# Kernel optimization log

Measured on AMD Instinct MI355X. Metric: run time of the kernel, lower is better.

Reference implementation:

```python
import jax, jax.numpy as jnp
import numpy as np


def setup_inputs() -> dict:
    key = jax.random.key(0)
    k1, k2, k3, k4, k5 = jax.random.split(key, 5)
    B, C, H, W = 8, 32, 64, 64
    inp = jax.random.normal(k1, (B, C, H, W), dtype=jnp.float32)
    # expected positions lie inside the image grid
    exPx = jax.random.uniform(k2, (B, H, W), dtype=jnp.float32) * (W - 1)
    exPy = jax.random.uniform(k3, (B, H, W), dtype=jnp.float32) * (H - 1)
    # positive Gaussian widths in roughly [1, 3]
    sigmax = jax.random.uniform(k4, (B, H, W), dtype=jnp.float32) * 2.0 + 1.0
    sigmay = jax.random.uniform(k5, (B, H, W), dtype=jnp.float32) * 2.0 + 1.0
    return {"input": inp, "exPx": exPx, "exPy": exPy,
            "sigmax": sigmax, "sigmay": sigmay}


def reference(input, exPx, exPy, sigmax, sigmay):
    """Gaussian-weighted spatial swap/warp (soft gather).

    For each output pixel (i, j):
      out[b,c,i,j] = sum_{u,v} G(u; exPy[b,i,j], sigmay[b,i,j])
                              * G(v; exPx[b,i,j], sigmax[b,i,j])
                              * input[b,c,u,v]  /  Z[b,i,j]
    where G is an unnormalized Gaussian and Z is the total weight mass.
    The 2D Gaussian weight is separable, so we contract rows then cols.
    """
    B, C, H, W = input.shape
    u = jnp.arange(H, dtype=input.dtype)  # source row coords (y)
    v = jnp.arange(W, dtype=input.dtype)  # source col coords (x)
    # wy: [B,H,W,H] weight over source rows u for each output pixel (i,j)
    wy = jnp.exp(-0.5 * ((u[None, None, None, :] - exPy[..., None]) / sigmay[..., None]) ** 2)
    # wx: [B,H,W,W] weight over source cols v
    wx = jnp.exp(-0.5 * ((v[None, None, None, :] - exPx[..., None]) / sigmax[..., None]) ** 2)
    # normalization mass per output pixel
    Z = wy.sum(-1) * wx.sum(-1) + jnp.asarray(1e-8, input.dtype)  # [B,H,W]
    # contract over source rows u -> [B,C,H,W,W]
    t = jnp.einsum('biju,bcuv->bcijv', wy, input)
    # contract over source cols v -> [B,C,H,W]
    out = jnp.einsum('bcijv,bijv->bcij', t, wx)
    return out / Z[:, None]
```

## Files before the change

### kernel.cpp

```cpp
#include <hip/hip_runtime.h>


#define BB 8
#define CC 32
#define HH 64
#define WW 64

typedef __attribute__((ext_vector_type(8))) short short8;
typedef __attribute__((ext_vector_type(4))) float f32x4;
typedef unsigned int uint;

__device__ __forceinline__ uint rn_bf16(float f) {
    uint u = __float_as_uint(f);
    return (u + 0x7FFFu + ((u >> 16) & 1u)) >> 16;
}

__global__ void preconvert_kernel(const float* __restrict__ x, uint* __restrict__ hi)
{
    const int n = BB * CC * HH * WW / 2;
    int idx = blockIdx.x * blockDim.x + threadIdx.x;
    for (; idx < n; idx += gridDim.x * blockDim.x) {
        const float2 d = ((const float2*)x)[idx];
        hi[idx] = rn_bf16(d.x) | (rn_bf16(d.y) << 16);
    }
}

#define WYB_OFF   0
#define WXH_OFF   8704
#define SUM_OFF   17920
#define INVZ_OFF  19968
#define LDS_BYTES 20224
#define RED_OFF   0

__global__ __launch_bounds__(256, 6)
void swap_mfma_kernel(const uint* __restrict__ xhi,
                      const float* __restrict__ exPx, const float* __restrict__ exPy,
                      const float* __restrict__ sigmax, const float* __restrict__ sigmay,
                      float* __restrict__ out)
{
    __shared__ __align__(16) char lds[LDS_BYTES];
    const int t    = threadIdx.x;
    const int lane = t & 63;
    const int w    = t >> 6;
    const int q    = (t >> 4) & 3;
    const int ln   = t & 15;
    const int bid   = blockIdx.x;
    const int b     = bid & 7;
    const int r     = bid >> 3;
    const int chalf = r & 1;
    const int i     = r >> 1;
    const int bi    = b * 64 + i;

    {
        const int p = lane;
        const int g = w;
        const int pixBase = bi * 64 + p;
        const float ey = exPy[pixBase], ex = exPx[pixBase];
        const float isy = 1.0f / sigmay[pixBase], isx = 1.0f / sigmax[pixBase];
        float sy = 0.0f, sx = 0.0f;
        uint* WYB = (uint*)(lds + WYB_OFF);
        #pragma unroll
        for (int j = 0; j < 8; ++j) {
            const int u0 = g * 16 + 2 * j;
            const float dy0 = ((float)u0       - ey) * isy;
            const float dy1 = ((float)(u0 + 1) - ey) * isy;
            const float wy0 = __expf(-0.5f * dy0 * dy0);
            const float wy1 = __expf(-0.5f * dy1 * dy1);
            sy += wy0 + wy1;
            WYB[p * 34 + g * 8 + j] = rn_bf16(wy0) | (rn_bf16(wy1) << 16);
        }
        uint* WXH = (uint*)(lds + WXH_OFF);
        #pragma unroll
        for (int j = 0; j < 8; ++j) {
            const int v0 = g * 16 + 2 * j;
            const float dx0 = ((float)v0       - ex) * isx;
            const float dx1 = ((float)(v0 + 1) - ex) * isx;
            const float wx0 = __expf(-0.5f * dx0 * dx0);
            const float wx1 = __expf(-0.5f * dx1 * dx1);
            sx += wx0 + wx1;
            WXH[p * 36 + g * 8 + j] = rn_bf16(wx0) | (rn_bf16(wx1) << 16);
        }
        float* SUMY = (float*)(lds + SUM_OFF);
        float* SUMX = SUMY + 256;
        SUMY[g * 64 + p] = sy;
        SUMX[g * 64 + p] = sx;
    }
    __syncthreads();
    float* INVZ = (float*)(lds + INVZ_OFF);
    if (t < 64) {
        float* SUMY = (float*)(lds + SUM_OFF);
        float* SUMX = SUMY + 256;
        const float sy = SUMY[t] + SUMY[64 + t] + SUMY[128 + t] + SUMY[192 + t];
        const float sx = SUMX[t] + SUMX[64 + t] + SUMX[128 + t] + SUMX[192 + t];
        INVZ[t] = 1.0f / (sy * sx + 1e-8f);
    }
    __syncthreads();

    short8 bh[4][2];
    #pragma unroll
    for (int nt = 0; nt < 4; ++nt)
        #pragma unroll
        for (int ks = 0; ks < 2; ++ks)
            bh[nt][ks] = *(const short8*)(lds + WXH_OFF + (nt * 16 + ln) * 144 + ks * 64 + q * 16);
    float wyz[4][4];
    #pragma unroll
    for (int nt = 0; nt < 4; ++nt) {
        const int pp = nt * 16 + ln;
        const float iz = INVZ[pp];
        const uint2 wv = *(const uint2*)((const uint*)(lds + WYB_OFF) + pp * 34 + w * 8 + q * 2);
        wyz[nt][0] = __uint_as_float(wv.x << 16)          * iz;
        wyz[nt][1] = __uint_as_float(wv.x & 0xFFFF0000u)  * iz;
        wyz[nt][2] = __uint_as_float(wv.y << 16)          * iz;
        wyz[nt][3] = __uint_as_float(wv.y & 0xFFFF0000u)  * iz;
    }
    __syncthreads();

    const int cbase = b * CC + chalf * 16;
    float* RED = (float*)(lds + RED_OFF);
    const uint* xrow = xhi + (size_t)cbase * 2048 + (w * 16 + ln) * 32 + q * 4;

    #pragma unroll 4
    for (int c = 0; c < 16; ++c) {
        const uint4* src = (const uint4*)(xrow + (size_t)c * 2048);
        union { uint4 v; short8 s; } A0, A1;
        A0.v = src[0];
        A1.v = src[4];

        f32x4 acc[4];
        #pragma unroll
        for (int nt = 0; nt < 4; ++nt) acc[nt] = (f32x4){0.f, 0.f, 0.f, 0.f};
        #pragma unroll
        for (int nt = 0; nt < 4; ++nt) {
            acc[nt] = __builtin_amdgcn_mfma_f32_16x16x32_bf16(A0.s, bh[nt][0], acc[nt], 0, 0, 0);
            acc[nt] = __builtin_amdgcn_mfma_f32_16x16x32_bf16(A1.s, bh[nt][1], acc[nt], 0, 0, 0);
        }
        #pragma unroll
        for (int nt = 0; nt < 4; ++nt) {
            float ps = acc[nt][0] * wyz[nt][0] + acc[nt][1] * wyz[nt][1]
                     + acc[nt][2] * wyz[nt][2] + acc[nt][3] * wyz[nt][3];
            ps += __shfl_xor(ps, 16, 64);
            ps += __shfl_xor(ps, 32, 64);
            if (q == 0) RED[c * 256 + w * 64 + nt * 16 + ln] = ps;
        }
    }
    __syncthreads();

    {
        const int kk = t >> 6, p = t & 63;
        #pragma unroll
        for (int g = 0; g < 4; ++g) {
            const int c = g * 4 + kk;
            const float* Rk = RED + c * 256;
            const float o = Rk[p] + Rk[64 + p] + Rk[128 + p] + Rk[192 + p];
            out[(size_t)(cbase + c) * (HH * WW) + i * 64 + p] = o;
        }
    }
}

__device__ __forceinline__ void split_pair(float f0, float f1, uint& hi, uint& lo) {
    const uint u0 = __float_as_uint(f0), u1 = __float_as_uint(f1);
    hi = (u0 >> 16) | (u1 & 0xFFFF0000u);
    const float l0 = f0 - __uint_as_float(u0 & 0xFFFF0000u);
    const float l1 = f1 - __uint_as_float(u1 & 0xFFFF0000u);
    lo = (__float_as_uint(l0) >> 16) | (__float_as_uint(l1) & 0xFFFF0000u);
}

#define FB_WYS_OFF   0
#define FB_WXH_OFF   16640
#define FB_SUM_OFF   25856
#define FB_INVZ_OFF  27904
#define FB_LDS_BYTES 28160
#define FB_RED_OFF   0

__global__ __launch_bounds__(256, 4)
void swap_fused_kernel(const float* __restrict__ inp,
                       const float* __restrict__ exPx, const float* __restrict__ exPy,
                       const float* __restrict__ sigmax, const float* __restrict__ sigmay,
                       float* __restrict__ out)
{
    __shared__ __align__(16) char lds[FB_LDS_BYTES];
    const int t = threadIdx.x;
    const int lane = t & 63, w = t >> 6, q = (t >> 4) & 3, ln = t & 15;
    const int bid = blockIdx.x;
    const int b = bid & 7, r = bid >> 3;
    const int chalf = r & 1, i = r >> 1;
    const int bi = b * 64 + i;

    float* WYS = (float*)(lds + FB_WYS_OFF);
    {
        const int p = lane, g = w;
        const int pixBase = bi * 64 + p;
        const float ey = exPy[pixBase], ex = exPx[pixBase];
        const float isy = 1.0f / sigmay[pixBase], isx = 1.0f / sigmax[pixBase];
        float sy = 0.0f, sx = 0.0f;
        #pragma unroll
        for (int k = 0; k < 16; ++k) {
            const int u = g * 16 + k;
            const float dy = ((float)u - ey) * isy;
            const float wy = __expf(-0.5f * dy * dy);
            WYS[u * 65 + p] = wy; sy += wy;
        }
        uint* WXH = (uint*)(lds + FB_WXH_OFF);
        #pragma unroll
        for (int j = 0; j < 8; ++j) {
            const int v0 = g * 16 + 2 * j;
            const float dx0 = ((float)v0 - ex) * isx;
            const float dx1 = ((float)(v0 + 1) - ex) * isx;
            const float wx0 = __expf(-0.5f * dx0 * dx0);
            const float wx1 = __expf(-0.5f * dx1 * dx1);
            sx += wx0 + wx1;
            WXH[p * 36 + g * 8 + j] = rn_bf16(wx0) | (rn_bf16(wx1) << 16);
        }
        float* SUMY = (float*)(lds + FB_SUM_OFF);
        float* SUMX = SUMY + 256;
        SUMY[g * 64 + p] = sy; SUMX[g * 64 + p] = sx;
    }
    __syncthreads();
    float* INVZ = (float*)(lds + FB_INVZ_OFF);
    if (t < 64) {
        float* SUMY = (float*)(lds + FB_SUM_OFF);
        float* SUMX = SUMY + 256;
        const float sy = SUMY[t] + SUMY[64 + t] + SUMY[128 + t] + SUMY[192 + t];
        const float sx = SUMX[t] + SUMX[64 + t] + SUMX[128 + t] + SUMX[192 + t];
        INVZ[t] = 1.0f / (sy * sx + 1e-8f);
    }
    __syncthreads();
    short8 bh[4][2];
    #pragma unroll
    for (int nt = 0; nt < 4; ++nt)
        #pragma unroll
        for (int ks = 0; ks < 2; ++ks)
            bh[nt][ks] = *(const short8*)(lds + FB_WXH_OFF + (nt * 16 + ln) * 144 + ks * 64 + q * 16);
    float wyz[4][4];
    #pragma unroll
    for (int nt = 0; nt < 4; ++nt) {
        const float iz = INVZ[nt * 16 + ln];
        #pragma unroll
        for (int rr = 0; rr < 4; ++rr)
            wyz[nt][rr] = WYS[(w * 16 + q * 4 + rr) * 65 + nt * 16 + ln] * iz;
    }
    __syncthreads();
    const int cbase = b * CC + chalf * 16;
    float* RED = (float*)(lds + FB_RED_OFF);
    const float* xrow = inp + (size_t)cbase * 4096 + (w * 16 + ln) * 64 + q * 8;
    #pragma unroll 2
    for (int c = 0; c < 16; ++c) {
        const float4* src = (const float4*)(xrow + (size_t)c * 4096);
        const float4 x0 = src[0], x1 = src[1], x2 = src[8], x3 = src[9];
        union { uint u[4]; short8 s; } Ah0, Al0, Ah1, Al1;
        split_pair(x0.x, x0.y, Ah0.u[0], Al0.u[0]);
        split_pair(x0.z, x0.w, Ah0.u[1], Al0.u[1]);
        split_pair(x1.x, x1.y, Ah0.u[2], Al0.u[2]);
        split_pair(x1.z, x1.w, Ah0.u[3], Al0.u[3]);
        split_pair(x2.x, x2.y, Ah1.u[0], Al1.u[0]);
        split_pair(x2.z, x2.w, Ah1.u[1], Al1.u[1]);
        split_pair(x3.x, x3.y, Ah1.u[2], Al1.u[2]);
        split_pair(x3.z, x3.w, Ah1.u[3], Al1.u[3]);
        f32x4 acc[4];
        #pragma unroll
        for (int nt = 0; nt < 4; ++nt) acc[nt] = (f32x4){0.f, 0.f, 0.f, 0.f};
        #pragma unroll
        for (int nt = 0; nt < 4; ++nt) {
            acc[nt] = __builtin_amdgcn_mfma_f32_16x16x32_bf16(Ah0.s, bh[nt][0], acc[nt], 0, 0, 0);
            acc[nt] = __builtin_amdgcn_mfma_f32_16x16x32_bf16(Al0.s, bh[nt][0], acc[nt], 0, 0, 0);
            acc[nt] = __builtin_amdgcn_mfma_f32_16x16x32_bf16(Ah1.s, bh[nt][1], acc[nt], 0, 0, 0);
            acc[nt] = __builtin_amdgcn_mfma_f32_16x16x32_bf16(Al1.s, bh[nt][1], acc[nt], 0, 0, 0);
        }
        #pragma unroll
        for (int nt = 0; nt < 4; ++nt) {
            float ps = acc[nt][0] * wyz[nt][0] + acc[nt][1] * wyz[nt][1]
                     + acc[nt][2] * wyz[nt][2] + acc[nt][3] * wyz[nt][3];
            ps += __shfl_xor(ps, 16, 64);
            ps += __shfl_xor(ps, 32, 64);
            if (q == 0) RED[c * 256 + w * 64 + nt * 16 + ln] = ps;
        }
    }
    __syncthreads();
    {
        const int kk = t >> 6, p = t & 63;
        #pragma unroll
        for (int g = 0; g < 4; ++g) {
            const int c = g * 4 + kk;
            const float* Rk = RED + c * 256;
            const float o = Rk[p] + Rk[64 + p] + Rk[128 + p] + Rk[192 + p];
            out[(size_t)(cbase + c) * (HH * WW) + i * 64 + p] = o;
        }
    }
}

extern "C" void kernel_launch(void* const* d_in, const int* in_sizes, int n_in,
                              void* d_out, int out_size, void* d_ws, size_t ws_size,
                              hipStream_t stream) {
    const float* inp    = (const float*)d_in[0];
    const float* exPx   = (const float*)d_in[1];
    const float* exPy   = (const float*)d_in[2];
    const float* sigmax = (const float*)d_in[3];
    const float* sigmay = (const float*)d_in[4];
    float* out = (float*)d_out;

    const size_t plane_bytes = (size_t)BB * CC * HH * WW * 2;
    if (ws_size >= plane_bytes) {
        uint* xhi = (uint*)d_ws;
        hipLaunchKernelGGL(preconvert_kernel, dim3(1024), dim3(256), 0, stream, inp, xhi);
        hipLaunchKernelGGL(swap_mfma_kernel, dim3(BB * HH * 2), dim3(256), 0, stream,
                           xhi, exPx, exPy, sigmax, sigmay, out);
    } else {
        hipLaunchKernelGGL(swap_fused_kernel, dim3(BB * HH * 2), dim3(256), 0, stream,
                           inp, exPx, exPy, sigmax, sigmay, out);
    }
}
```

Before: 89.29 us.

## Split channels across waves and prefetch bf16 input tiles through a register ring

Each wave now owns four channels and loops over all 64 source rows itself, so the per-channel reduction across waves through LDS and the trailing barrier and reduction pass go away. Input loads are issued early, before the weight setup, and held in a three-deep register ring so global latency overlaps the MFMA work. The y-weights for all row tiles are kept in registers and the 1/Z normalisation is applied once at the final store. In exchange register use grows, so the launch-bounds occupancy hint drops from 6 to 4 blocks per CU.

New measurement: 90.71 us. Within noise of the previous version (+1.6%).

```diff
diff --git a/kernel.cpp b/kernel.cpp
--- a/kernel.cpp
+++ b/kernel.cpp
@@ -30,9 +30,8 @@
 #define SUM_OFF   17920
 #define INVZ_OFF  19968
 #define LDS_BYTES 20224
-#define RED_OFF   0
-
-__global__ __launch_bounds__(256, 6)
+
+__global__ __launch_bounds__(256, 4)
 void swap_mfma_kernel(const uint* __restrict__ xhi,
                       const float* __restrict__ exPx, const float* __restrict__ exPy,
                       const float* __restrict__ sigmax, const float* __restrict__ sigmay,
@@ -51,6 +50,17 @@
     const int i     = r >> 1;
     const int bi    = b * 64 + i;
 
+    const int cplane0 = b * CC + chalf * 16 + w * 4;
+    const uint* xbase = xhi + (size_t)cplane0 * 2048 + ln * 32 + q * 4;
+    union AU { uint4 v; short8 s; };
+    AU abuf[3][2];
+    #pragma unroll
+    for (int s = 0; s < 3; ++s) {
+        const uint* xs = xbase + s * 512;
+        abuf[s][0].v = *(const uint4*)(xs);
+        abuf[s][1].v = *(const uint4*)(xs + 16);
+    }
+
     {
         const int p = lane;
         const int g = w;
@@ -102,58 +112,57 @@
         #pragma unroll
         for (int ks = 0; ks < 2; ++ks)
             bh[nt][ks] = *(const short8*)(lds + WXH_OFF + (nt * 16 + ln) * 144 + ks * 64 + q * 16);
-    float wyz[4][4];
+    uint2 wyb[4][4];
     #pragma unroll
     for (int nt = 0; nt < 4; ++nt) {
         const int pp = nt * 16 + ln;
-        const float iz = INVZ[pp];
-        const uint2 wv = *(const uint2*)((const uint*)(lds + WYB_OFF) + pp * 34 + w * 8 + q * 2);
-        wyz[nt][0] = __uint_as_float(wv.x << 16)          * iz;
-        wyz[nt][1] = __uint_as_float(wv.x & 0xFFFF0000u)  * iz;
-        wyz[nt][2] = __uint_as_float(wv.y << 16)          * iz;
-        wyz[nt][3] = __uint_as_float(wv.y & 0xFFFF0000u)  * iz;
-    }
-    __syncthreads();
-
-    const int cbase = b * CC + chalf * 16;
-    float* RED = (float*)(lds + RED_OFF);
-    const uint* xrow = xhi + (size_t)cbase * 2048 + (w * 16 + ln) * 32 + q * 4;
-
-    #pragma unroll 4
-    for (int c = 0; c < 16; ++c) {
-        const uint4* src = (const uint4*)(xrow + (size_t)c * 2048);
-        union { uint4 v; short8 s; } A0, A1;
-        A0.v = src[0];
-        A1.v = src[4];
-
-        f32x4 acc[4];
-        #pragma unroll
-        for (int nt = 0; nt < 4; ++nt) acc[nt] = (f32x4){0.f, 0.f, 0.f, 0.f};
+        #pragma unroll
+        for (int mt = 0; mt < 4; ++mt)
+            wyb[mt][nt] = *(const uint2*)((const uint*)(lds + WYB_OFF) + pp * 34 + mt * 8 + q * 2);
+    }
+    const float invzL = INVZ[lane];
+
+    float* obase = out + (size_t)cplane0 * 4096 + i * 64 + lane;
+
+    #pragma unroll
+    for (int c = 0; c < 4; ++c) {
+        float ps[4] = {0.f, 0.f, 0.f, 0.f};
+        #pragma unroll
+        for (int mt = 0; mt < 4; ++mt) {
+            const int s = c * 4 + mt;
+            const short8 a0 = abuf[s % 3][0].s;
+            const short8 a1 = abuf[s % 3][1].s;
+
+            f32x4 acc[4];
+            #pragma unroll
+            for (int nt = 0; nt < 4; ++nt) acc[nt] = (f32x4){0.f, 0.f, 0.f, 0.f};
+            #pragma unroll
+            for (int nt = 0; nt < 4; ++nt) {
+                acc[nt] = __builtin_amdgcn_mfma_f32_16x16x32_bf16(a0, bh[nt][0], acc[nt], 0, 0, 0);
+                acc[nt] = __builtin_amdgcn_mfma_f32_16x16x32_bf16(a1, bh[nt][1], acc[nt], 0, 0, 0);
+            }
+            if (s + 3 < 16) {
+                const int sn = s + 3;
+                const uint* xs = xbase + (sn >> 2) * 2048 + (sn & 3) * 512;
+                abuf[s % 3][0].v = *(const uint4*)(xs);
+                abuf[s % 3][1].v = *(const uint4*)(xs + 16);
+            }
+            #pragma unroll
+            for (int nt = 0; nt < 4; ++nt) {
+                const uint2 wv = wyb[mt][nt];
+                ps[nt] += acc[nt][0] * __uint_as_float(wv.x << 16)
+                        + acc[nt][1] * __uint_as_float(wv.x & 0xFFFF0000u)
+                        + acc[nt][2] * __uint_as_float(wv.y << 16)
+                        + acc[nt][3] * __uint_as_float(wv.y & 0xFFFF0000u);
+            }
+        }
         #pragma unroll
         for (int nt = 0; nt < 4; ++nt) {
-            acc[nt] = __builtin_amdgcn_mfma_f32_16x16x32_bf16(A0.s, bh[nt][0], acc[nt], 0, 0, 0);
-            acc[nt] = __builtin_amdgcn_mfma_f32_16x16x32_bf16(A1.s, bh[nt][1], acc[nt], 0, 0, 0);
-        }
-        #pragma unroll
-        for (int nt = 0; nt < 4; ++nt) {
-            float ps = acc[nt][0] * wyz[nt][0] + acc[nt][1] * wyz[nt][1]
-                     + acc[nt][2] * wyz[nt][2] + acc[nt][3] * wyz[nt][3];
-            ps += __shfl_xor(ps, 16, 64);
-            ps += __shfl_xor(ps, 32, 64);
-            if (q == 0) RED[c * 256 + w * 64 + nt * 16 + ln] = ps;
-        }
-    }
-    __syncthreads();
-
-    {
-        const int kk = t >> 6, p = t & 63;
-        #pragma unroll
-        for (int g = 0; g < 4; ++g) {
-            const int c = g * 4 + kk;
-            const float* Rk = RED + c * 256;
-            const float o = Rk[p] + Rk[64 + p] + Rk[128 + p] + Rk[192 + p];
-            out[(size_t)(cbase + c) * (HH * WW) + i * 64 + p] = o;
-        }
+            ps[nt] += __shfl_xor(ps[nt], 16, 64);
+            ps[nt] += __shfl_xor(ps[nt], 32, 64);
+        }
+        const float po = (q == 0) ? ps[0] : (q == 1) ? ps[1] : (q == 2) ? ps[2] : ps[3];
+        obase[(size_t)c * 4096] = po * invzL;
     }
 }
 
```
